# Optimization experiments

Measured on AMD Instinct MI355X. Metric: run time of the kernel, lower is better.

The kernel has to match this reference:

```python
import jax, jax.numpy as jnp
import numpy as np

B, L, IN_DIM, D, H, NCONV = 64, 400, 500, 128, 8, 4
HD = D // H  # head dim = 16


def _conv1d(x, w, b, pad, groups=1):
    # x: [B, L, Cin], w: [k, Cin//groups, Cout]
    y = jax.lax.conv_general_dilated(
        x, w, window_strides=(1,), padding=[(pad, pad)],
        dimension_numbers=('NWC', 'WIO', 'NWC'), feature_group_count=groups)
    return y + b


def _layernorm(x, g, b, eps=1e-5):
    mu = jnp.mean(x, axis=-1, keepdims=True)
    var = jnp.mean(jnp.square(x - mu), axis=-1, keepdims=True)
    return (x - mu) * jax.lax.rsqrt(var + eps) * g + b


def _posenc(L, d):
    pos = jnp.arange(L, dtype=jnp.float32)[:, None]                 # [L,1]
    div = jnp.exp(jnp.arange(0, d, 2, dtype=jnp.float32) * (-jnp.log(10000.0) / d))
    ang = pos * div                                                 # [L, d/2]
    return jnp.stack([jnp.sin(ang), jnp.cos(ang)], axis=-1).reshape(L, d)


def setup_inputs() -> dict:
    key = jax.random.key(0)
    ks = jax.random.split(key, 24)
    s = lambda k, shape, scale: jax.random.normal(k, shape, dtype=jnp.float32) * scale
    inp = {
        'x': s(ks[0], (B, L, IN_DIM), 1.0),
        # init conv: k=5, 500 -> 128
        'w_init': s(ks[1], (5, IN_DIM, D), 0.02),
        'b_init': jnp.zeros((D,), jnp.float32),
        # 4 depthwise-separable conv layers (pre-LN, residual): depthwise k=7
        'ln_conv_g': jnp.ones((NCONV, D), jnp.float32),
        'ln_conv_b': jnp.zeros((NCONV, D), jnp.float32),
        'w_dw': s(ks[2], (NCONV, 7, 1, D), 0.1),
        'b_dw': jnp.zeros((NCONV, D), jnp.float32),
        'w_pw': s(ks[3], (NCONV, 1, D, D), 0.05),
        'b_pw': jnp.zeros((NCONV, D), jnp.float32),
        # self-attention (pre-LN, residual)
        'ln_att_g': jnp.ones((D,), jnp.float32),
        'ln_att_b': jnp.zeros((D,), jnp.float32),
        'wq': s(ks[4], (D, D), 0.05), 'bq': jnp.zeros((D,), jnp.float32),
        'wk': s(ks[5], (D, D), 0.05), 'bk': jnp.zeros((D,), jnp.float32),
        'wv': s(ks[6], (D, D), 0.05), 'bv': jnp.zeros((D,), jnp.float32),
        'wo': s(ks[7], (D, D), 0.05), 'bo': jnp.zeros((D,), jnp.float32),
        # FFN (pre-LN, residual)
        'ln_ffn_g': jnp.ones((D,), jnp.float32),
        'ln_ffn_b': jnp.zeros((D,), jnp.float32),
        'w1': s(ks[8], (D, D), 0.05), 'b1': jnp.zeros((D,), jnp.float32),
        'w2': s(ks[9], (D, D), 0.05), 'b2': jnp.zeros((D,), jnp.float32),
    }
    return inp


def reference(x, w_init, b_init, ln_conv_g, ln_conv_b, w_dw, b_dw, w_pw, b_pw,
              ln_att_g, ln_att_b, wq, bq, wk, bk, wv, bv, wo, bo,
              ln_ffn_g, ln_ffn_b, w1, b1, w2, b2):
    # 1) init conv (Conv1d k=5 pad=2, 500 -> 128); torch permutes, equivalent NWC conv
    h = _conv1d(x, w_init, b_init, pad=2)                    # [B, L, D]
    # 2) positional encoding
    h = h + _posenc(h.shape[1], D)
    for i in range(NCONV):
        res = h
        h = _layernorm(h, ln_conv_g[i], ln_conv_b[i])
        h = _conv1d(h, w_dw[i], b_dw[i], pad=3, groups=D)    # depthwise k=7
        h = _conv1d(h, w_pw[i], b_pw[i], pad=0)              # pointwise 1x1
        h = jax.nn.relu(h) + res
    # 4) multi-head self-attention, pre-LN + residual
    res = h
    hn = _layernorm(h, ln_att_g, ln_att_b)
    q = (hn @ wq + bq).reshape(B, L, H, HD)
    k = (hn @ wk + bk).reshape(B, L, H, HD)
    v = (hn @ wv + bv).reshape(B, L, H, HD)
    scores = jnp.einsum('bqhd,bkhd->bhqk', q, k) / jnp.sqrt(jnp.float32(HD))
    attn = jax.nn.softmax(scores, axis=-1)
    o = jnp.einsum('bhqk,bkhd->bqhd', attn, v).reshape(B, L, D)
    h = o @ wo + bo + res
    # 5) FFN, pre-LN + residual
    res = h
    hn = _layernorm(h, ln_ffn_g, ln_ffn_b)
    h = jax.nn.relu(hn @ w1 + b1) @ w2 + b2 + res
    return h
```

## Files before the change

### kernel.cpp

```cpp
#include <hip/hip_runtime.h>
#include <hip/hip_bf16.h>
#include <math.h>

#define B 64
#define L 400
#define IN_DIM 500
#define D 128
#define H 8
#define HD 16
#define NCONV 4
#define BL (B*L)

typedef __attribute__((ext_vector_type(8))) unsigned short ushort8;
typedef __attribute__((ext_vector_type(8))) short bf16x8;
typedef __attribute__((ext_vector_type(4))) float f32x4;

__device__ __forceinline__ unsigned short f2bf(float f) {
    unsigned u = __float_as_uint(f);
    unsigned r = (u + 0x7fffu + ((u >> 16) & 1u)) >> 16;
    return (unsigned short)r;
}
__device__ __forceinline__ float bf2f(unsigned short u) {
    return __uint_as_float(((unsigned)u) << 16);
}
__device__ __forceinline__ unsigned cvtpk_bf16(float lo, float hi) {
    unsigned r;
    asm("v_cvt_pk_bf16_f32 %0, %1, %2" : "=v"(r) : "v"(lo), "v"(hi));
    return r;
}

__device__ __forceinline__ void gload16(const void* g, void* l) {
    __builtin_amdgcn_global_load_lds(
        (const __attribute__((address_space(1))) unsigned int*)g,
        (__attribute__((address_space(3))) unsigned int*)l,
        16, 0, 0);
}

__global__ __launch_bounds__(256) void k_cvt_all(
        const float* __restrict__ x, unsigned short* __restrict__ xb,
        const float* __restrict__ w_init, unsigned short* __restrict__ wbt,
        const float* __restrict__ w_pw, const float* __restrict__ wq,
        const float* __restrict__ wk, const float* __restrict__ wv,
        const float* __restrict__ wo, const float* __restrict__ w1,
        const float* __restrict__ w2, unsigned short* __restrict__ wt) {
    int bid = blockIdx.x;
    if (bid < 6464) {
        int idx = bid * 256 + threadIdx.x;
        int row = idx >> 6, ch = idx & 63;
        int b = row / 404, rr = row - b * 404;
        ushort8 o = (ushort8)0;
        if (rr >= 2 && rr < 402) {
            int l = rr - 2;
            const float* src = x + ((size_t)b * 400 + l) * 500 + ch * 8;
            if (ch < 62) {
                float4 v0 = *(const float4*)(src);
                float4 v1 = *(const float4*)(src + 4);
                o[0] = f2bf(v0.x); o[1] = f2bf(v0.y); o[2] = f2bf(v0.z); o[3] = f2bf(v0.w);
                o[4] = f2bf(v1.x); o[5] = f2bf(v1.y); o[6] = f2bf(v1.z); o[7] = f2bf(v1.w);
            } else {
#pragma unroll
                for (int j = 0; j < 8; ++j) {
                    int c = ch * 8 + j;
                    o[j] = (c < 500) ? f2bf(src[j]) : (unsigned short)0;
                }
            }
        }
        *(ushort8*)(xb + (size_t)idx * 8) = o;
    } else if (bid < 7744) {
        int idx = (bid - 6464) * 256 + threadIdx.x;
        int k = idx & 511, n = (idx >> 9) & 127, t = idx >> 16;
        float v = (k < 500) ? w_init[((size_t)t * 500 + k) * 128 + n] : 0.f;
        wbt[idx] = f2bf(v);
    } else {
        int rb = bid - 7744;
        const float* arr[10] = {w_pw, w_pw + 16384, w_pw + 2 * 16384,
                                w_pw + 3 * 16384, wq, wk, wv, wo, w1, w2};
        int widx = rb >> 6;
        const float* w = arr[widx];
        int idx = ((rb & 63) << 8) + threadIdx.x;
        int n = idx >> 7, k = idx & 127;
        wt[(size_t)widx * 16384 + idx] = f2bf(w[k * 128 + n]);
    }
}

#define TM 80
#define BK 64
__global__ __launch_bounds__(256) void k_initconv_mfma(
        const unsigned short* __restrict__ xb,
        const unsigned short* __restrict__ wbt,
        const float* __restrict__ bias, float* __restrict__ out) {
    __shared__ unsigned short As[84 * BK];
    __shared__ unsigned short Ws[5][64 * BK];
    int tid = threadIdx.x;
    int b = blockIdx.x / 10;
    int rem = blockIdx.x - b * 10;
    int l0 = (rem >> 1) * TM;
    int nh = rem & 1;
    int lane = tid & 63, wave = tid >> 6;
    int kgrp = lane >> 4, lm = lane & 15;

    f32x4 acc[5];
#pragma unroll
    for (int mf = 0; mf < 5; ++mf) acc[mf] = (f32x4)0.f;

    const unsigned short* abase = xb + ((size_t)(b * 404 + l0)) * 512;
    const unsigned short* wbase = wbt + (size_t)nh * 64 * 512;

    for (int k0 = 0; k0 < 512; k0 += BK) {
        for (int idx = tid; idx < 672; idx += 256) {
            int r = idx >> 3, sc = idx & 7;
            gload16(abase + (size_t)r * 512 + k0 + ((sc ^ (r & 7)) * 8),
                    As + idx * 8);
        }
#pragma unroll
        for (int i = 0; i < 10; ++i) {
            int idx = tid + i * 256;
            int t = idx >> 9;
            int sub = idx & 511;
            int n = sub >> 3, sc = sub & 7;
            gload16(wbase + (size_t)t * 128 * 512 + (size_t)n * 512 + k0
                        + ((sc ^ (n & 7)) * 8),
                    &Ws[t][0] + sub * 8);
        }
        __syncthreads();
        int n16 = wave * 16 + lm;
#pragma unroll
        for (int ks = 0; ks < 2; ++ks) {
            int gc = ks * 4 + kgrp;
            bf16x8 bfr[5];
#pragma unroll
            for (int t = 0; t < 5; ++t)
                bfr[t] = *(const bf16x8*)(&Ws[t][0] + n16 * 64
                                          + ((gc ^ (n16 & 7)) * 8));
#pragma unroll
            for (int mf = 0; mf < 5; ++mf) {
#pragma unroll
                for (int t = 0; t < 5; ++t) {
                    int r = mf * 16 + lm + t;
                    bf16x8 af = *(const bf16x8*)(As + r * 64
                                                 + ((gc ^ (r & 7)) * 8));
                    acc[mf] = __builtin_amdgcn_mfma_f32_16x16x32_bf16(
                        af, bfr[t], acc[mf], 0, 0, 0);
                }
            }
        }
        __syncthreads();
    }

    {
        int n = nh * 64 + wave * 16 + lm;
        float bs = bias[n];
        float pbase = expf(-(float)(n & ~1) * (9.210340371976184f / 128.0f));
#pragma unroll
        for (int mf = 0; mf < 5; ++mf) {
#pragma unroll
            for (int r = 0; r < 4; ++r) {
                int l = l0 + mf * 16 + kgrp * 4 + r;
                float ang = (float)l * pbase;
                float pe = (n & 1) ? cosf(ang) : sinf(ang);
                out[((size_t)b * 400 + l) * 128 + n] = acc[mf][r] + bs + pe;
            }
        }
    }
}

#define CB_ROWS 38
__global__ __launch_bounds__(256) void k_convblock(
        const float* __restrict__ hin, float* __restrict__ hout,
        const float* __restrict__ lng, const float* __restrict__ lnb,
        const float* __restrict__ wdw, const float* __restrict__ bdw,
        const unsigned short* __restrict__ wpt, const float* __restrict__ bpw) {
    __shared__ unsigned short Ws[128 * 128];
    __shared__ unsigned short Ln[CB_ROWS * 128];
    __shared__ unsigned short Dw[32 * 128];
    int tid = threadIdx.x;
    int b = blockIdx.x / 13;
    int tile = blockIdx.x - b * 13;
    int l0 = tile * 32;
    int lv = (l0 + 32 <= L) ? 32 : (L - l0);
    int lane = tid & 63, wave = tid >> 6;
    int lm = lane & 15, kgrp = lane >> 4;

#pragma unroll
    for (int i = 0; i < 8; ++i) {
        int idx = tid + i * 256;
        int n = idx >> 4, sc = idx & 15;
        gload16(wpt + (size_t)n * 128 + ((sc ^ (n & 15)) * 8), Ws + idx * 8);
    }

    {
        float2 gg = *(const float2*)(lng + lane * 2);
        float2 bb = *(const float2*)(lnb + lane * 2);
#pragma unroll
        for (int ri = 0; ri < 10; ++ri) {
            int r = wave + ri * 4;
            if (r < CB_ROWS) {
                int gl = l0 - 3 + r;
                bool ok = (gl >= 0 && gl < L);
                float2 v = make_float2(0.f, 0.f);
                if (ok) v = *(const float2*)(hin + ((size_t)b * L + gl) * 128 + lane * 2);
                float s = v.x + v.y;
                float q = v.x * v.x + v.y * v.y;
#pragma unroll
                for (int off = 32; off; off >>= 1) {
                    s += __shfl_xor(s, off);
                    q += __shfl_xor(q, off);
                }
                float mu  = s * (1.f / 128.f);
                float var = q * (1.f / 128.f) - mu * mu;
                float inv = rsqrtf(var + 1e-5f);
                unsigned pk = 0;
                if (ok) {
                    float ox = (v.x - mu) * inv * gg.x + bb.x;
                    float oy = (v.y - mu) * inv * gg.y + bb.y;
                    pk = (unsigned)f2bf(ox) | ((unsigned)f2bf(oy) << 16);
                }
                *(unsigned*)(Ln + r * 128 + lane * 2) = pk;
            }
        }
    }
    __syncthreads();

    {
        int d = tid & 127, half = tid >> 7;
        float wr[7];
#pragma unroll
        for (int t = 0; t < 7; ++t) wr[t] = wdw[t * 128 + d];
        float bs = bdw[d];
        float win[7];
#pragma unroll
        for (int t = 0; t < 6; ++t) win[t] = bf2f(Ln[(half * 16 + t) * 128 + d]);
#pragma unroll
        for (int lj = 0; lj < 16; ++lj) {
            int l = half * 16 + lj;
            win[6] = bf2f(Ln[(l + 6) * 128 + d]);
            float a = bs;
#pragma unroll
            for (int t = 0; t < 7; ++t) a = fmaf(win[t], wr[t], a);
#pragma unroll
            for (int t = 0; t < 6; ++t) win[t] = win[t + 1];
            Dw[l * 128 + ((d >> 3) ^ (l & 15)) * 8 + (d & 7)] = f2bf(a);
        }
    }
    __syncthreads();

    f32x4 acc[2][2];
#pragma unroll
    for (int mf = 0; mf < 2; ++mf)
#pragma unroll
        for (int nt = 0; nt < 2; ++nt) acc[mf][nt] = (f32x4)0.f;
#pragma unroll
    for (int kc = 0; kc < 4; ++kc) {
        int c = kc * 4 + kgrp;
        bf16x8 af[2];
#pragma unroll
        for (int mf = 0; mf < 2; ++mf) {
            int r = mf * 16 + lm;
            af[mf] = *(const bf16x8*)(Dw + r * 128 + (c ^ (r & 15)) * 8);
        }
#pragma unroll
        for (int nt = 0; nt < 2; ++nt) {
            int n = wave * 32 + nt * 16 + lm;
            bf16x8 bfv = *(const bf16x8*)(Ws + n * 128 + (c ^ (n & 15)) * 8);
#pragma unroll
            for (int mf = 0; mf < 2; ++mf)
                acc[mf][nt] = __builtin_amdgcn_mfma_f32_16x16x32_bf16(
                    af[mf], bfv, acc[mf][nt], 0, 0, 0);
        }
    }

#pragma unroll
    for (int nt = 0; nt < 2; ++nt) {
        int n = wave * 32 + nt * 16 + lm;
        float bsn = bpw[n];
#pragma unroll
        for (int mf = 0; mf < 2; ++mf) {
#pragma unroll
            for (int r = 0; r < 4; ++r) {
                int row = mf * 16 + kgrp * 4 + r;
                if (row < lv) {
                    size_t gi = ((size_t)b * L + l0 + row) * 128 + n;
                    hout[gi] = fmaxf(acc[mf][nt][r] + bsn, 0.f) + hin[gi];
                }
            }
        }
    }
}

__global__ __launch_bounds__(256) void k_ln_gemm(
        const float* __restrict__ h, const float* __restrict__ g,
        const float* __restrict__ bta, const unsigned short* __restrict__ wt0,
        int nw, const float* __restrict__ bias0, const float* __restrict__ bias1,
        const float* __restrict__ bias2, unsigned short* __restrict__ out0,
        unsigned short* __restrict__ out1, unsigned short* __restrict__ out2,
        float s0, int relu) {
    __shared__ unsigned short As[32 * 128];
    __shared__ unsigned short Ws[128 * 128];
    int tid = threadIdx.x;
    int m0 = blockIdx.x * 32;
    int lane = tid & 63, wave = tid >> 6;
    int lm = lane & 15, kgrp = lane >> 4;
    int wm = wave >> 1, wn = wave & 1;

#pragma unroll
    for (int i = 0; i < 8; ++i) {
        int idx = tid + i * 256;
        int n = idx >> 4, sc = idx & 15;
        gload16(wt0 + (size_t)n * 128 + ((sc ^ (n & 15)) * 8), Ws + idx * 8);
    }

    {
        float2 gg = *(const float2*)(g + lane * 2);
        float2 bb = *(const float2*)(bta + lane * 2);
#pragma unroll
        for (int ri = 0; ri < 8; ++ri) {
            int r = wave + ri * 4;
            float2 v = *(const float2*)(h + ((size_t)m0 + r) * 128 + lane * 2);
            float s = v.x + v.y;
            float q = v.x * v.x + v.y * v.y;
#pragma unroll
            for (int off = 32; off; off >>= 1) {
                s += __shfl_xor(s, off);
                q += __shfl_xor(q, off);
            }
            float mu  = s * (1.f / 128.f);
            float var = q * (1.f / 128.f) - mu * mu;
            float inv = rsqrtf(var + 1e-5f);
            float ox = (v.x - mu) * inv * gg.x + bb.x;
            float oy = (v.y - mu) * inv * gg.y + bb.y;
            unsigned pk = (unsigned)f2bf(ox) | ((unsigned)f2bf(oy) << 16);
            *(unsigned*)(As + r * 128 + ((lane >> 2) ^ (r & 15)) * 8
                         + ((lane * 2) & 7)) = pk;
        }
    }

    for (int i = 0; i < nw; ++i) {
        __syncthreads();
        f32x4 acc[4];
#pragma unroll
        for (int nt = 0; nt < 4; ++nt) acc[nt] = (f32x4)0.f;
#pragma unroll
        for (int kc = 0; kc < 4; ++kc) {
            int c = kc * 4 + kgrp;
            int r = wm * 16 + lm;
            bf16x8 af = *(const bf16x8*)(As + r * 128 + (c ^ (r & 15)) * 8);
#pragma unroll
            for (int nt = 0; nt < 4; ++nt) {
                int n = wn * 64 + nt * 16 + lm;
                bf16x8 bfv = *(const bf16x8*)(Ws + n * 128 + (c ^ (n & 15)) * 8);
                acc[nt] = __builtin_amdgcn_mfma_f32_16x16x32_bf16(
                    af, bfv, acc[nt], 0, 0, 0);
            }
        }
        const float* bias = (i == 0) ? bias0 : (i == 1) ? bias1 : bias2;
        unsigned short* out = (i == 0) ? out0 : (i == 1) ? out1 : out2;
        float sc0 = (i == 0) ? s0 : 1.f;
#pragma unroll
        for (int nt = 0; nt < 4; ++nt) {
            int n = wn * 64 + nt * 16 + lm;
            float bsn = bias[n];
#pragma unroll
            for (int r = 0; r < 4; ++r) {
                size_t m = (size_t)m0 + wm * 16 + kgrp * 4 + r;
                float v = acc[nt][r] + bsn;
                if (relu) v = fmaxf(v, 0.f);
                out[m * 128 + n] = f2bf(v * sc0);
            }
        }
        if (i + 1 < nw) {
            __syncthreads();
            const unsigned short* wp = wt0 + (size_t)(i + 1) * 16384;
#pragma unroll
            for (int j = 0; j < 8; ++j) {
                int idx = tid + j * 256;
                int n = idx >> 4, sc = idx & 15;
                gload16(wp + (size_t)n * 128 + ((sc ^ (n & 15)) * 8), Ws + idx * 8);
            }
        }
    }
}

__global__ __launch_bounds__(256) void k_oproj_ffn(
        const unsigned short* __restrict__ A,
        const float* __restrict__ res,
        const unsigned short* __restrict__ wot, const float* __restrict__ bo,
        const float* __restrict__ lng, const float* __restrict__ lnb,
        const unsigned short* __restrict__ w1t, const float* __restrict__ b1,
        const unsigned short* __restrict__ w2t, const float* __restrict__ b2,
        float* __restrict__ outp) {
    __shared__ unsigned short Ws[128 * 128];
    __shared__ unsigned short As[32 * 128];
    __shared__ float Hm[32 * 128];
    __shared__ unsigned short Mid[32 * 128];
    int tid = threadIdx.x;
    int m0 = blockIdx.x * 32;
    int lane = tid & 63, wave = tid >> 6;
    int lm = lane & 15, kgrp = lane >> 4;
    int wm = wave >> 1, wn = wave & 1;

#pragma unroll
    for (int i = 0; i < 8; ++i) {
        int idx = tid + i * 256;
        int n = idx >> 4, sc = idx & 15;
        gload16(wot + (size_t)n * 128 + ((sc ^ (n & 15)) * 8), Ws + idx * 8);
    }
#pragma unroll
    for (int i = 0; i < 2; ++i) {
        int idx = tid + i * 256;
        int r = idx >> 4, sc = idx & 15;
        gload16(A + ((size_t)(m0 + r)) * 128 + ((sc ^ (r & 15)) * 8), As + idx * 8);
    }
    __syncthreads();

    {
        f32x4 acc[4];
#pragma unroll
        for (int nt = 0; nt < 4; ++nt) acc[nt] = (f32x4)0.f;
#pragma unroll
        for (int kc = 0; kc < 4; ++kc) {
            int c = kc * 4 + kgrp;
            int r = wm * 16 + lm;
            bf16x8 af = *(const bf16x8*)(As + (r * 16 + (c ^ (r & 15))) * 8);
#pragma unroll
            for (int nt = 0; nt < 4; ++nt) {
                int n = wn * 64 + nt * 16 + lm;
                bf16x8 bfv = *(const bf16x8*)(Ws + (n * 16 + (c ^ (n & 15))) * 8);
                acc[nt] = __builtin_amdgcn_mfma_f32_16x16x32_bf16(af, bfv, acc[nt], 0, 0, 0);
            }
        }
#pragma unroll
        for (int nt = 0; nt < 4; ++nt) {
            int n = wn * 64 + nt * 16 + lm;
            float bsn = bo[n];
#pragma unroll
            for (int r = 0; r < 4; ++r) {
                int row = wm * 16 + kgrp * 4 + r;
                Hm[row * 128 + n] = acc[nt][r] + bsn
                                    + res[((size_t)m0 + row) * 128 + n];
            }
        }
    }
    __syncthreads();

#pragma unroll
    for (int i = 0; i < 8; ++i) {
        int idx = tid + i * 256;
        int n = idx >> 4, sc = idx & 15;
        gload16(w1t + (size_t)n * 128 + ((sc ^ (n & 15)) * 8), Ws + idx * 8);
    }
    {
        float2 gg = *(const float2*)(lng + lane * 2);
        float2 bb = *(const float2*)(lnb + lane * 2);
#pragma unroll
        for (int ri = 0; ri < 8; ++ri) {
            int r = wave + ri * 4;
            float2 v = *(const float2*)(Hm + r * 128 + lane * 2);
            float s = v.x + v.y;
            float q = v.x * v.x + v.y * v.y;
#pragma unroll
            for (int off = 32; off; off >>= 1) {
                s += __shfl_xor(s, off);
                q += __shfl_xor(q, off);
            }
            float mu  = s * (1.f / 128.f);
            float var = q * (1.f / 128.f) - mu * mu;
            float inv = rsqrtf(var + 1e-5f);
            float ox = (v.x - mu) * inv * gg.x + bb.x;
            float oy = (v.y - mu) * inv * gg.y + bb.y;
            unsigned pk = (unsigned)f2bf(ox) | ((unsigned)f2bf(oy) << 16);
            *(unsigned*)(As + r * 128 + ((lane >> 2) ^ (r & 15)) * 8
                         + ((lane * 2) & 7)) = pk;
        }
    }
    __syncthreads();

    {
        f32x4 acc[4];
#pragma unroll
        for (int nt = 0; nt < 4; ++nt) acc[nt] = (f32x4)0.f;
#pragma unroll
        for (int kc = 0; kc < 4; ++kc) {
            int c = kc * 4 + kgrp;
            int r = wm * 16 + lm;
            bf16x8 af = *(const bf16x8*)(As + (r * 16 + (c ^ (r & 15))) * 8);
#pragma unroll
            for (int nt = 0; nt < 4; ++nt) {
                int n = wn * 64 + nt * 16 + lm;
                bf16x8 bfv = *(const bf16x8*)(Ws + (n * 16 + (c ^ (n & 15))) * 8);
                acc[nt] = __builtin_amdgcn_mfma_f32_16x16x32_bf16(af, bfv, acc[nt], 0, 0, 0);
            }
        }
#pragma unroll
        for (int nt = 0; nt < 4; ++nt) {
            int n = wn * 64 + nt * 16 + lm;
            float bsn = b1[n];
#pragma unroll
            for (int r = 0; r < 4; ++r) {
                int row = wm * 16 + kgrp * 4 + r;
                float v = fmaxf(acc[nt][r] + bsn, 0.f);
                Mid[row * 128 + ((n >> 3) ^ (row & 15)) * 8 + (n & 7)] = f2bf(v);
            }
        }
    }
    __syncthreads();

#pragma unroll
    for (int i = 0; i < 8; ++i) {
        int idx = tid + i * 256;
        int n = idx >> 4, sc = idx & 15;
        gload16(w2t + (size_t)n * 128 + ((sc ^ (n & 15)) * 8), Ws + idx * 8);
    }
    __syncthreads();

    {
        f32x4 acc[4];
#pragma unroll
        for (int nt = 0; nt < 4; ++nt) acc[nt] = (f32x4)0.f;
#pragma unroll
        for (int kc = 0; kc < 4; ++kc) {
            int c = kc * 4 + kgrp;
            int r = wm * 16 + lm;
            bf16x8 af = *(const bf16x8*)(Mid + (r * 16 + (c ^ (r & 15))) * 8);
#pragma unroll
            for (int nt = 0; nt < 4; ++nt) {
                int n = wn * 64 + nt * 16 + lm;
                bf16x8 bfv = *(const bf16x8*)(Ws + (n * 16 + (c ^ (n & 15))) * 8);
                acc[nt] = __builtin_amdgcn_mfma_f32_16x16x32_bf16(af, bfv, acc[nt], 0, 0, 0);
            }
        }
#pragma unroll
        for (int nt = 0; nt < 4; ++nt) {
            int n = wn * 64 + nt * 16 + lm;
            float bsn = b2[n];
#pragma unroll
            for (int r = 0; r < 4; ++r) {
                int row = wm * 16 + kgrp * 4 + r;
                outp[((size_t)m0 + row) * 128 + n] =
                    acc[nt][r] + bsn + Hm[row * 128 + n];
            }
        }
    }
}

#define KS 40
#define VS 424
#define PSZ (16 * KS)
__global__ __launch_bounds__(512) void k_attn_mfma(
        const unsigned short* __restrict__ qb,
        const unsigned short* __restrict__ kb,
        const unsigned short* __restrict__ vb,
        unsigned short* __restrict__ out) {
    __shared__ __align__(16) unsigned short Kpad[400 * KS];
    __shared__ __align__(16) unsigned short Vt[16 * VS];
    __shared__ __align__(16) unsigned short Ptmp[8][2 * PSZ];
    int tid = threadIdx.x;
    int b = blockIdx.x & 63, h = blockIdx.x >> 6;
    int lane = tid & 63, wave = tid >> 6;
    int lm = lane & 15, g = lane >> 4;

    for (int idx = tid; idx < 800; idx += 512) {
        int l = idx >> 1, half = idx & 1;
        ushort8 kv = *(const ushort8*)(kb + ((size_t)(b * 400 + l)) * 128 + h * 16 + half * 8);
        *(ushort8*)(Kpad + l * KS + half * 8) = kv;
        *(ushort8*)(Kpad + l * KS + 16 + half * 8) = (ushort8)0;
    }
    for (int idx = tid; idx < 800; idx += 512) {
        int kk = idx >> 1, dh = idx & 1;
        ushort8 vv = *(const ushort8*)(vb + ((size_t)(b * 400 + kk)) * 128 + h * 16 + dh * 8);
#pragma unroll
        for (int j = 0; j < 8; ++j) Vt[(dh * 8 + j) * VS + kk] = vv[j];
    }
    if (tid < 256) {
        int d = tid >> 4, kk = 400 + (tid & 15);
        Vt[d * VS + kk] = 0;
    }
    __syncthreads();

    unsigned short* Pw = Ptmp[wave];
    for (int tt = wave; tt < 25; tt += 8) {
        int q0 = tt * 16;
        bf16x8 Qf = *(const bf16x8*)(qb + ((size_t)(b * 400 + q0 + lm)) * 128 + h * 16 + g * 8);
        f32x4 s[25];
        __builtin_amdgcn_s_setprio(1);
#pragma unroll
        for (int kt = 0; kt < 25; ++kt) {
            bf16x8 Kf = *(const bf16x8*)(Kpad + (kt * 16 + lm) * KS + g * 8);
            s[kt] = __builtin_amdgcn_mfma_f32_16x16x32_bf16(Kf, Qf, (f32x4)0.f, 0, 0, 0);
        }
        __builtin_amdgcn_s_setprio(0);
        float m = -1e30f;
#pragma unroll
        for (int kt = 0; kt < 25; ++kt)
            m = fmaxf(m, fmaxf(fmaxf(s[kt][0], s[kt][1]),
                               fmaxf(s[kt][2], s[kt][3])));
        m = fmaxf(m, __shfl_xor(m, 16));
        m = fmaxf(m, __shfl_xor(m, 32));

        f32x4 O = (f32x4)0.f;
        f32x4 sumv = (f32x4)0.f;

        {
            f32x4 p;
            p[0] = __expf(s[0][0] - m);
            p[1] = __expf(s[0][1] - m);
            p[2] = __expf(s[0][2] - m);
            p[3] = __expf(s[0][3] - m);
            sumv += p;
            uint2 w; w.x = cvtpk_bf16(p[0], p[1]); w.y = cvtpk_bf16(p[2], p[3]);
            *(uint2*)(Pw + lm * KS + g * 4) = w;
            f32x4 p2;
            p2[0] = __expf(s[1][0] - m);
            p2[1] = __expf(s[1][1] - m);
            p2[2] = __expf(s[1][2] - m);
            p2[3] = __expf(s[1][3] - m);
            sumv += p2;
            uint2 w2; w2.x = cvtpk_bf16(p2[0], p2[1]); w2.y = cvtpk_bf16(p2[2], p2[3]);
            *(uint2*)(Pw + lm * KS + 16 + g * 4) = w2;
        }

#pragma unroll
        for (int kc = 0; kc < 13; ++kc) {
            unsigned short* cur = Pw + (kc & 1) * PSZ;
            bf16x8 Pf = *(const bf16x8*)(cur + lm * KS + g * 8);
            bf16x8 Vf = *(const bf16x8*)(Vt + lm * VS + kc * 32 + g * 8);
            if (kc < 12) {
                unsigned short* nxt = Pw + ((kc + 1) & 1) * PSZ;
                {
                    int kt = 2 * (kc + 1);
                    f32x4 p;
                    p[0] = __expf(s[kt][0] - m);
                    p[1] = __expf(s[kt][1] - m);
                    p[2] = __expf(s[kt][2] - m);
                    p[3] = __expf(s[kt][3] - m);
                    sumv += p;
                    uint2 w; w.x = cvtpk_bf16(p[0], p[1]); w.y = cvtpk_bf16(p[2], p[3]);
                    *(uint2*)(nxt + lm * KS + g * 4) = w;
                }
                {
                    int kt = 2 * (kc + 1) + 1;
                    uint2 w; w.x = 0u; w.y = 0u;
                    if (kt < 25) {
                        f32x4 p;
                        p[0] = __expf(s[kt][0] - m);
                        p[1] = __expf(s[kt][1] - m);
                        p[2] = __expf(s[kt][2] - m);
                        p[3] = __expf(s[kt][3] - m);
                        sumv += p;
                        w.x = cvtpk_bf16(p[0], p[1]); w.y = cvtpk_bf16(p[2], p[3]);
                    }
                    *(uint2*)(nxt + lm * KS + 16 + g * 4) = w;
                }
            }
            O = __builtin_amdgcn_mfma_f32_16x16x32_bf16(Pf, Vf, O, 0, 0, 0);
        }
        float sum = (sumv[0] + sumv[1]) + (sumv[2] + sumv[3]);
        sum += __shfl_xor(sum, 16);
        sum += __shfl_xor(sum, 32);
        float rinv = 1.f / sum;
#pragma unroll
        for (int r = 0; r < 4; ++r) {
            float rq = __shfl(rinv, g * 4 + r);
            int q = q0 + g * 4 + r;
            out[((size_t)(b * 400 + q)) * 128 + h * 16 + lm] = f2bf(O[r] * rq);
        }
    }
}

extern "C" void kernel_launch(void* const* d_in, const int* in_sizes, int n_in,
                              void* d_out, int out_size, void* d_ws, size_t ws_size,
                              hipStream_t stream) {
    (void)in_sizes; (void)n_in; (void)out_size; (void)ws_size;
    const float* x      = (const float*)d_in[0];
    const float* w_init = (const float*)d_in[1];
    const float* b_init = (const float*)d_in[2];
    const float* lncg   = (const float*)d_in[3];
    const float* lncb   = (const float*)d_in[4];
    const float* w_dw   = (const float*)d_in[5];
    const float* b_dw   = (const float*)d_in[6];
    const float* w_pw   = (const float*)d_in[7];
    const float* b_pw   = (const float*)d_in[8];
    const float* lnag   = (const float*)d_in[9];
    const float* lnab   = (const float*)d_in[10];
    const float* wq     = (const float*)d_in[11];
    const float* bq     = (const float*)d_in[12];
    const float* wk     = (const float*)d_in[13];
    const float* bk     = (const float*)d_in[14];
    const float* wv     = (const float*)d_in[15];
    const float* bv     = (const float*)d_in[16];
    const float* wo     = (const float*)d_in[17];
    const float* bo     = (const float*)d_in[18];
    const float* lnfg   = (const float*)d_in[19];
    const float* lnfb   = (const float*)d_in[20];
    const float* w1     = (const float*)d_in[21];
    const float* b1     = (const float*)d_in[22];
    const float* w2     = (const float*)d_in[23];
    const float* b2     = (const float*)d_in[24];

    float* ws = (float*)d_ws;
    const size_t NBL = (size_t)BL * D;
    float* h0 = ws;
    float* outp = (float*)d_out;

    unsigned short* hnb = (unsigned short*)(ws + NBL);
    unsigned short* t0b = hnb + NBL;
    unsigned short* qb  = t0b + NBL;
    unsigned short* kb  = qb + NBL;
    unsigned short* vb  = kb + NBL;
    unsigned short* wt  = vb + NBL;
    unsigned short* xb  = wt + 10 * 16384;
    unsigned short* wbt = xb + (size_t)64 * 404 * 512;
    float* h1 = (float*)(wbt + (size_t)5 * 128 * 512);

    k_cvt_all<<<8384, 256, 0, stream>>>(x, xb, w_init, wbt,
                                        w_pw, wq, wk, wv, wo, w1, w2, wt);

    k_initconv_mfma<<<640, 256, 0, stream>>>(xb, wbt, b_init, h0);

    for (int i = 0; i < NCONV; ++i) {
        const float* hin = (i & 1) ? h1 : h0;
        float* hout      = (i & 1) ? h0 : h1;
        k_convblock<<<832, 256, 0, stream>>>(
            hin, hout, lncg + i * D, lncb + i * D,
            w_dw + (size_t)i * 7 * D, b_dw + i * D,
            wt + (size_t)i * 16384, b_pw + i * D);
    }

    k_ln_gemm<<<800, 256, 0, stream>>>(h0, lnag, lnab, wt + 4 * 16384, 3,
                                       bq, bk, bv, qb, kb, vb, 0.25f, 0);
    k_attn_mfma<<<512, 512, 0, stream>>>(qb, kb, vb, t0b);

    k_oproj_ffn<<<800, 256, 0, stream>>>(
        t0b, h0, wt + 7 * 16384, bo, lnfg, lnfb,
        wt + 8 * 16384, b1, wt + 9 * 16384, b2, outp);
}
```

Before: 305.9 us.

## Double-buffer input tile in LDS and read init-conv weights directly from global

The init-conv MFMA kernel now double-buffers the activation tile in shared memory, prefetching the next K-chunk while computing the current one. This needs only one barrier per iteration instead of two. Weight fragments are no longer staged through LDS; each lane loads its bf16x8 B fragments straight from global memory, cutting LDS use and the weight copy. The trade-off is more global (L2) traffic and latency exposure on the weight loads, which are not prefetched. Whether gload16 is an async direct-to-LDS load affects how much overlap the prefetch actually gives.

```diff
diff --git a/kernel.cpp b/kernel.cpp
--- a/kernel.cpp
+++ b/kernel.cpp
@@ -89,8 +89,7 @@
         const unsigned short* __restrict__ xb,
         const unsigned short* __restrict__ wbt,
         const float* __restrict__ bias, float* __restrict__ out) {
-    __shared__ unsigned short As[84 * BK];
-    __shared__ unsigned short Ws[5][64 * BK];
+    __shared__ unsigned short As[2][84 * BK];
     int tid = threadIdx.x;
     int b = blockIdx.x / 10;
     int rem = blockIdx.x - b * 10;
@@ -104,47 +103,44 @@
     for (int mf = 0; mf < 5; ++mf) acc[mf] = (f32x4)0.f;
 
     const unsigned short* abase = xb + ((size_t)(b * 404 + l0)) * 512;
-    const unsigned short* wbase = wbt + (size_t)nh * 64 * 512;
-
+    const unsigned short* wn = wbt + (size_t)(nh * 64 + wave * 16 + lm) * 512;
+
+    for (int idx = tid; idx < 672; idx += 256) {
+        int r = idx >> 3, sc = idx & 7;
+        gload16(abase + (size_t)r * 512 + ((sc ^ (r & 7)) * 8), As[0] + idx * 8);
+    }
+
+    int cur = 0;
     for (int k0 = 0; k0 < 512; k0 += BK) {
-        for (int idx = tid; idx < 672; idx += 256) {
-            int r = idx >> 3, sc = idx & 7;
-            gload16(abase + (size_t)r * 512 + k0 + ((sc ^ (r & 7)) * 8),
-                    As + idx * 8);
-        }
-#pragma unroll
-        for (int i = 0; i < 10; ++i) {
-            int idx = tid + i * 256;
-            int t = idx >> 9;
-            int sub = idx & 511;
-            int n = sub >> 3, sc = sub & 7;
-            gload16(wbase + (size_t)t * 128 * 512 + (size_t)n * 512 + k0
-                        + ((sc ^ (n & 7)) * 8),
-                    &Ws[t][0] + sub * 8);
-        }
         __syncthreads();
-        int n16 = wave * 16 + lm;
+        if (k0 + BK < 512) {
+            int nk = k0 + BK;
+            for (int idx = tid; idx < 672; idx += 256) {
+                int r = idx >> 3, sc = idx & 7;
+                gload16(abase + (size_t)r * 512 + nk + ((sc ^ (r & 7)) * 8),
+                        As[cur ^ 1] + idx * 8);
+            }
+        }
 #pragma unroll
         for (int ks = 0; ks < 2; ++ks) {
             int gc = ks * 4 + kgrp;
             bf16x8 bfr[5];
 #pragma unroll
             for (int t = 0; t < 5; ++t)
-                bfr[t] = *(const bf16x8*)(&Ws[t][0] + n16 * 64
-                                          + ((gc ^ (n16 & 7)) * 8));
+                bfr[t] = *(const bf16x8*)(wn + (size_t)t * 65536 + k0 + gc * 8);
 #pragma unroll
             for (int mf = 0; mf < 5; ++mf) {
 #pragma unroll
                 for (int t = 0; t < 5; ++t) {
                     int r = mf * 16 + lm + t;
-                    bf16x8 af = *(const bf16x8*)(As + r * 64
+                    bf16x8 af = *(const bf16x8*)(As[cur] + r * 64
                                                  + ((gc ^ (r & 7)) * 8));
                     acc[mf] = __builtin_amdgcn_mfma_f32_16x16x32_bf16(
                         af, bfr[t], acc[mf], 0, 0, 0);
                 }
             }
         }
-        __syncthreads();
+        cur ^= 1;
     }
 
     {
```

New measurement: 318.8 us. +4.2%, slower.
